# Performance work log

Measured on AMD Instinct MI355X. Metric: run time of the kernel, lower is better.

The kernel has to match this reference:

```python
import math
import jax, jax.numpy as jnp
import numpy as np

B, T, C = 4, 2048, 1024
H = 16
HS = C // H  # head_size = 64

def setup_inputs() -> dict:
    key = jax.random.key(0)
    k1, k2, k3 = jax.random.split(key, 3)
    x = jax.random.normal(k1, (B, T, C), dtype=jnp.float32)
    W_qkv = jax.random.normal(k2, (C, 3 * C), dtype=jnp.float32) * (1.0 / math.sqrt(C))
    W_proj = jax.random.normal(k3, (C, C), dtype=jnp.float32) * (1.0 / math.sqrt(C))
    b_proj = jnp.zeros((C,), dtype=jnp.float32)
    return {"x": x, "W_qkv": W_qkv, "W_proj": W_proj, "b_proj": b_proj}

def reference(x, W_qkv, W_proj, b_proj):
    Bx, Tx, Cx = x.shape
    qkv = x @ W_qkv  # [B,T,3C]
    q, k, v = jnp.split(qkv, 3, axis=-1)
    # [B,T,C] -> [B,H,T,HS]
    def heads(t):
        return t.reshape(Bx, Tx, H, HS).transpose(0, 2, 1, 3)
    q, k, v = heads(q), heads(k), heads(v)
    scores = jnp.einsum('bhqd,bhkd->bhqk', q, k) / math.sqrt(HS)
    causal = jnp.tril(jnp.ones((Tx, Tx), dtype=bool))
    scores = jnp.where(causal, scores, -jnp.inf)
    attn = jax.nn.softmax(scores, axis=-1)
    out = jnp.einsum('bhqk,bhkd->bhqd', attn, v)  # [B,H,T,HS]
    out = out.transpose(0, 2, 1, 3).reshape(Bx, Tx, Cx)
    return out @ W_proj + b_proj
```

## Files before the change

kernel.cpp:

```cpp
#include <hip/hip_runtime.h>
#include <hip/hip_bf16.h>
#include <cstdint>
#include <cstddef>

using bf16 = __hip_bfloat16;
typedef __attribute__((ext_vector_type(8))) short short8;
typedef __attribute__((ext_vector_type(4))) float floatx4;

#define B_ 4
#define T_ 2048
#define C_ 1024
#define H_ 16
#define HS_ 64
#define BT_ (B_*T_)
#define N3C (3*C_)

#define MFMA16(a,b,c) __builtin_amdgcn_mfma_f32_16x16x32_bf16((a),(b),(c),0,0,0)

#if __has_builtin(__builtin_amdgcn_exp2f)
#define EXP2(x) __builtin_amdgcn_exp2f(x)
#else
#define EXP2(x) exp2f(x)
#endif

static __device__ __forceinline__ void gld16(const bf16* g, bf16* l) {
  __builtin_amdgcn_global_load_lds(
      (const __attribute__((address_space(1))) unsigned int*)g,
      (__attribute__((address_space(3))) unsigned int*)l, 16, 0, 0);
}

static __device__ __forceinline__ unsigned short f2bf_us(float x) {
  bf16 b = __float2bfloat16(x);
  return *(unsigned short*)&b;
}

__global__ __launch_bounds__(256)
void k_prep(const float* __restrict__ x, bf16* __restrict__ xb,
            const float* __restrict__ Wqkv, bf16* __restrict__ wqkvT,
            const float* __restrict__ Wproj, bf16* __restrict__ wprojT)
{
  const int bid = blockIdx.x, tid = threadIdx.x;
  __shared__ float tile[64][65];

  if (bid < 4096) {
    const int i = bid*256 + tid;
    const float4 v0 = ((const float4*)x)[2*i];
    const float4 v1 = ((const float4*)x)[2*i + 1];
    union { bf16 b[8]; uint4 u; } cvt;
    cvt.b[0] = __float2bfloat16(v0.x);
    cvt.b[1] = __float2bfloat16(v0.y);
    cvt.b[2] = __float2bfloat16(v0.z);
    cvt.b[3] = __float2bfloat16(v0.w);
    cvt.b[4] = __float2bfloat16(v1.x);
    cvt.b[5] = __float2bfloat16(v1.y);
    cvt.b[6] = __float2bfloat16(v1.z);
    cvt.b[7] = __float2bfloat16(v1.w);
    ((uint4*)xb)[i] = cvt.u;
    return;
  }

  const float* in; bf16* out; int N, n0, k0;
  if (bid < 4864) {
    const int j = bid - 4096;
    in = Wqkv; out = wqkvT; N = N3C;
    n0 = (j % 48) * 64; k0 = (j / 48) * 64;
  } else {
    const int j = bid - 4864;
    in = Wproj; out = wprojT; N = C_;
    n0 = (j % 16) * 64; k0 = (j / 16) * 64;
  }
  const int r = tid >> 6, c = tid & 63;
  #pragma unroll
  for (int j = 0; j < 16; ++j)
    tile[r + j*4][c] = in[(size_t)(k0 + r + j*4) * N + n0 + c];
  __syncthreads();
  #pragma unroll
  for (int j = 0; j < 16; ++j) {
    int rr = r + j*4;
    out[(size_t)(n0 + rr) * C_ + k0 + c] = __float2bfloat16(tile[c][rr]);
  }
}

template<int MODE, int NB>
__global__ __launch_bounds__(256, 2)
void k_gemm(const bf16* __restrict__ A, const bf16* __restrict__ Bt,
            int N, int K,
            bf16* __restrict__ Qb, bf16* __restrict__ Kb, bf16* __restrict__ Vt,
            float* __restrict__ Out, const float* __restrict__ bias)
{
  __shared__ __align__(16) char smem[65536];
  bf16* const sAb = (bf16*)smem;
  bf16* const sBb = (bf16*)(smem + 32768);

  const int tid  = threadIdx.x;
  const int lane = tid & 63, wave = tid >> 6;
  const int quad = lane >> 4, l16 = lane & 15;
  const int wm = wave >> 1, wn = wave & 1;

  const int g = blockIdx.x;
  const int xcd = g & 7;
  const int local = g >> 3;
  const int nb = local % NB;
  const int mb = (local / NB) * 8 + xcd;
  const int m0 = mb * 128, n0 = nb * 128;

  const int ra = tid >> 3;
  const int gc = (tid & 7) ^ (ra & 7);
  const bf16* aptr = A  + (size_t)(m0 + ra) * K + gc*8;
  const bf16* bptr = Bt + (size_t)(n0 + ra) * K + gc*8;
  const size_t rj = (size_t)32 * K;

  floatx4 acc[4][4] = {};
  const int KI = K >> 6;
  const int x7a = l16 & 7;

  for (int i = 0; i <= KI; ++i) {
    __syncthreads();
    if (i < KI) {
      const int k0 = i << 6;
      bf16* sa = sAb + (i & 1) * 8192;
      bf16* sb = sBb + (i & 1) * 8192;
      #pragma unroll
      for (int q2 = 0; q2 < 4; ++q2) {
        gld16(aptr + q2*rj + k0, sa + q2*2048 + tid*8);
        gld16(bptr + q2*rj + k0, sb + q2*2048 + tid*8);
      }
    }
    if (i == 0) continue;
    const bf16* sa = sAb + ((i-1) & 1) * 8192;
    const bf16* sb = sBb + ((i-1) & 1) * 8192;
    #pragma unroll
    for (int ks = 0; ks < 2; ++ks) {
      short8 af[4], bfm[4];
      #pragma unroll
      for (int ii = 0; ii < 4; ++ii)
        af[ii] = *(const short8*)&sa[(wm*64 + ii*16 + l16)*64 + ((ks*4 + quad) ^ x7a)*8];
      #pragma unroll
      for (int ii = 0; ii < 4; ++ii)
        bfm[ii] = *(const short8*)&sb[(wn*64 + ii*16 + l16)*64 + ((ks*4 + quad) ^ x7a)*8];
      #pragma unroll
      for (int ii = 0; ii < 4; ++ii)
        #pragma unroll
        for (int j = 0; j < 4; ++j)
          acc[ii][j] = MFMA16(af[ii], bfm[j], acc[ii][j]);
    }
  }

  if (MODE == 0 && nb >= 16) {
    __syncthreads();
    unsigned short* epi = (unsigned short*)smem;
    #pragma unroll
    for (int i = 0; i < 4; ++i) {
      const int tl = wm*64 + i*16 + quad*4;
      #pragma unroll
      for (int j = 0; j < 4; ++j) {
        const int ccl = wn*64 + j*16 + l16;
        #pragma unroll
        for (int r = 0; r < 4; ++r)
          epi[ccl*132 + tl + r] = f2bf_us(acc[i][j][r]);
      }
    }
    __syncthreads();
    const int b  = m0 >> 11;
    const int t0 = m0 & 2047;
    const int h0 = (n0 - 2*C_) >> 6;
    #pragma unroll
    for (int it = 0; it < 32; ++it) {
      const int id = it*256 + tid;
      const int tp = id & 31;
      const int rest = id >> 5;
      const int tl64 = (rest & 1) * 64;
      const int ccl = rest >> 1;
      const int k0p = tp + (tp & 16);
      const unsigned lo = epi[ccl*132 + tl64 + k0p];
      const unsigned hi = epi[ccl*132 + tl64 + k0p + 16];
      const int h = h0 + (ccl >> 6), d = ccl & 63;
      unsigned* row = (unsigned*)(Vt + ((size_t)(b*H_ + h) * HS_ + d) * T_);
      row[(t0 >> 1) + tl64/2 + tp] = lo | (hi << 16);
    }
  } else {
    #pragma unroll
    for (int i = 0; i < 4; ++i) {
      const int rowb = m0 + wm*64 + i*16 + quad*4;
      #pragma unroll
      for (int j = 0; j < 4; ++j) {
        const int col = n0 + wn*64 + j*16 + l16;
        #pragma unroll
        for (int r = 0; r < 4; ++r) {
          const float v = acc[i][j][r];
          const int rr = rowb + r;
          if (MODE == 0) {
            const int b = rr >> 11, t = rr & 2047;
            const int h = (col >> 6) & 15, d = col & 63;
            const size_t addr = (((size_t)(b*H_ + h) * T_ + t) << 6) + d;
            if (nb < 8) {
              Qb[addr] = __float2bfloat16(v * 0.18033688f);
            } else {
              Kb[addr] = __float2bfloat16(v);
            }
          } else {
            Out[(size_t)rr * N + col] = v + bias[col];
          }
        }
      }
    }
  }
}

__global__ __launch_bounds__(256, 2)
void k_attn(const bf16* __restrict__ Q, const bf16* __restrict__ K,
            const bf16* __restrict__ Vt, bf16* __restrict__ att)
{
  __shared__ bf16 kbuf[2][64*64];
  __shared__ bf16 vbuf[2][64*64];
  __shared__ bf16 pbuf[4][32*64];

  const int tid  = threadIdx.x;
  const int lane = tid & 63, wave = tid >> 6;
  const int quad = lane >> 4, l16 = lane & 15;
  const int x7 = l16 & 7;

  const int g  = blockIdx.x;
  const int bh = (g & 7) * 8 + (g >> 6);
  const int bx = (g >> 3) & 7;
  const int b = bh >> 4, h = bh & 15;

  const bf16* Qp = Q  + (size_t)bh * T_ * HS_;
  const bf16* Kp = K  + (size_t)bh * T_ * HS_;
  const bf16* Vp = Vt + (size_t)bh * HS_ * T_;

  const int qbase[2] = { (15-bx)*128 + wave*32, bx*128 + wave*32 };
  const int ntk0 = 32 - 2*bx;
  const int ntk1 = 2*bx + 2;

  short8 qf[2][2][2];
  #pragma unroll
  for (int t = 0; t < 2; ++t)
    #pragma unroll
    for (int mt = 0; mt < 2; ++mt)
      #pragma unroll
      for (int ss = 0; ss < 2; ++ss)
        qf[t][mt][ss] = *(const short8*)(Qp + (size_t)(qbase[t] + mt*16 + l16) * HS_ + ss*32 + quad*8);

  floatx4 o[2][2][4] = {};
  float lrow[2][2][4] = {};

  const bf16* kg[2]; const bf16* vg[2];
  int ldsoff[2];
  #pragma unroll
  for (int it = 0; it < 2; ++it) {
    const int c = it*256 + tid;
    const int row = c >> 3;
    const int col = (c & 7) ^ (row & 7);
    kg[it] = Kp + (size_t)row * HS_ + col*8;
    vg[it] = Vp + (size_t)row * T_ + col*8;
    ldsoff[it] = c*8;
  }

  bf16* pw = pbuf[wave];
  unsigned int* pw32 = (unsigned int*)pw;
  const int c0 = l16 >> 2;
  const int dwl = l16 & 3;

  for (int i = 0; i <= ntk0; ++i) {
    __syncthreads();
    if (i < ntk0) {
      const int stk0 = i * 64;
      bf16* kb = kbuf[i & 1];
      bf16* vb = vbuf[i & 1];
      #pragma unroll
      for (int it = 0; it < 2; ++it) {
        gld16(kg[it] + (size_t)stk0 * HS_, kb + ldsoff[it]);
        gld16(vg[it] + stk0,               vb + ldsoff[it]);
      }
    }
    if (i == 0) continue;
    const int tk  = i - 1;
    const int tk0 = tk * 64;
    const bf16* kb = kbuf[tk & 1];
    const bf16* vb = vbuf[tk & 1];

    #pragma unroll
    for (int t = 0; t < 2; ++t) {
      if (t == 1 && tk >= ntk1) break;
      if (tk0 > qbase[t] + 31) continue;

      floatx4 s[2][4] = {};
      #pragma unroll
      for (int nt = 0; nt < 4; ++nt) {
        const int key = nt*16 + l16;
        #pragma unroll
        for (int ss = 0; ss < 2; ++ss) {
          short8 kf = *(const short8*)&kb[(key*8 + ((ss*4+quad) ^ x7))*8];
          s[0][nt] = MFMA16(qf[t][0][ss], kf, s[0][nt]);
          s[1][nt] = MFMA16(qf[t][1][ss], kf, s[1][nt]);
        }
      }

      if (tk0 + 63 > qbase[t]) {
        #pragma unroll
        for (int mt = 0; mt < 2; ++mt)
          #pragma unroll
          for (int nt = 0; nt < 4; ++nt) {
            const int key = tk0 + nt*16 + l16;
            #pragma unroll
            for (int r = 0; r < 4; ++r) {
              const int qr = qbase[t] + mt*16 + quad*4 + r;
              if (key > qr) s[mt][nt][r] = -1e30f;
            }
          }
      }

      #pragma unroll
      for (int mt = 0; mt < 2; ++mt) {
        #pragma unroll
        for (int r = 0; r < 4; ++r) {
          const float p0 = EXP2(s[mt][0][r]), p1 = EXP2(s[mt][1][r]);
          const float p2 = EXP2(s[mt][2][r]), p3 = EXP2(s[mt][3][r]);
          lrow[t][mt][r] += (p0 + p1) + (p2 + p3);
          const int q = mt*16 + quad*4 + r;
          const unsigned w0 = __builtin_amdgcn_perm(__float_as_uint(p1), __float_as_uint(p0), 0x07060302u);
          const unsigned w1 = __builtin_amdgcn_perm(__float_as_uint(p3), __float_as_uint(p2), 0x07060302u);
          pw32[q*32 + (((c0 + q)     & 7) << 2) + dwl] = w0;
          pw32[q*32 + (((c0 + q + 4) & 7) << 2) + dwl] = w1;
        }
      }

      #pragma unroll
      for (int ss = 0; ss < 2; ++ss) {
        short8 pf0 = *(const short8*)&pw[l16*64      + ((4*ss + quad + l16) & 7)*8];
        short8 pf1 = *(const short8*)&pw[(16+l16)*64 + ((4*ss + quad + l16) & 7)*8];
        #pragma unroll
        for (int nd = 0; nd < 4; ++nd) {
          const int d = nd*16 + l16;
          short8 vf = *(const short8*)&vb[(d*8 + ((ss*4+quad) ^ x7))*8];
          o[t][0][nd] = MFMA16(pf0, vf, o[t][0][nd]);
          o[t][1][nd] = MFMA16(pf1, vf, o[t][1][nd]);
        }
      }
    }
  }

  #pragma unroll
  for (int t = 0; t < 2; ++t) {
    #pragma unroll
    for (int mt = 0; mt < 2; ++mt) {
      #pragma unroll
      for (int r = 0; r < 4; ++r) {
        float lsum = lrow[t][mt][r];
        lsum += __shfl_xor(lsum, 1);
        lsum += __shfl_xor(lsum, 2);
        lsum += __shfl_xor(lsum, 4);
        lsum += __shfl_xor(lsum, 8);
        const float inv = 1.0f / lsum;
        const int tt = qbase[t] + mt*16 + quad*4 + r;
        #pragma unroll
        for (int nd = 0; nd < 4; ++nd)
          att[(size_t)(b*T_ + tt) * C_ + h*64 + nd*16 + l16] =
              __float2bfloat16(o[t][mt][nd][r] * inv);
      }
    }
  }
}

extern "C" void kernel_launch(void* const* d_in, const int* in_sizes, int n_in,
                              void* d_out, int out_size, void* d_ws, size_t ws_size,
                              hipStream_t stream) {
  const float* x     = (const float*)d_in[0];
  const float* Wqkv  = (const float*)d_in[1];
  const float* Wproj = (const float*)d_in[2];
  const float* bproj = (const float*)d_in[3];
  float* out = (float*)d_out;

  char* ws = (char*)d_ws;
  bf16* xb     = (bf16*)(ws + 0);
  bf16* wqkvT  = (bf16*)(ws + 16777216);
  bf16* wprojT = (bf16*)(ws + 23068672);
  bf16* Qb     = (bf16*)(ws + 25165824);
  bf16* Kb     = (bf16*)(ws + 41943040);
  bf16* Vt     = (bf16*)(ws + 58720256);
  bf16* att    = (bf16*)(ws + 75497472);

  k_prep<<<dim3(5120), 256, 0, stream>>>(x, xb, Wqkv, wqkvT, Wproj, wprojT);
  k_gemm<0, 24><<<dim3(1536), 256, 0, stream>>>(
      xb, wqkvT, N3C, C_, Qb, Kb, Vt, nullptr, nullptr);
  k_attn<<<dim3(512), 256, 0, stream>>>(Qb, Kb, Vt, att);
  k_gemm<1, 8><<<dim3(512), 256, 0, stream>>>(
      att, wprojT, C_, C_, nullptr, nullptr, nullptr, out, bproj);
}
```

Baseline: 234.7 us.

## Split paired causal attention tiles into one tile per block, heaviest first

The attention kernel previously gave each block two paired query tiles (one long, one short) to balance causal work. Now each block handles a single 128-row query tile, the grid doubles to 1024 blocks, and blocks are ordered so the longest tiles are scheduled first. Register state is halved, so launch bounds are raised to allow three blocks per CU, and s_setprio wraps the MFMA sections to favour matrix issue across waves. The risk is more K/V reloads across blocks and tail imbalance if the heavy-first ordering does not hold in hardware scheduling.

```diff
diff --git a/kernel.cpp b/kernel.cpp
--- a/kernel.cpp
+++ b/kernel.cpp
@@ -207,7 +207,7 @@
   }
 }
 
-__global__ __launch_bounds__(256, 2)
+__global__ __launch_bounds__(256, 3)
 void k_attn(const bf16* __restrict__ Q, const bf16* __restrict__ K,
             const bf16* __restrict__ Vt, bf16* __restrict__ att)
 {
@@ -221,29 +221,26 @@
   const int x7 = l16 & 7;
 
   const int g  = blockIdx.x;
-  const int bh = (g & 7) * 8 + (g >> 6);
-  const int bx = (g >> 3) & 7;
+  const int bh = (g & 7) * 8 + ((g >> 3) & 7);
+  const int qt = 15 - (g >> 6);
   const int b = bh >> 4, h = bh & 15;
 
   const bf16* Qp = Q  + (size_t)bh * T_ * HS_;
   const bf16* Kp = K  + (size_t)bh * T_ * HS_;
   const bf16* Vp = Vt + (size_t)bh * HS_ * T_;
 
-  const int qbase[2] = { (15-bx)*128 + wave*32, bx*128 + wave*32 };
-  const int ntk0 = 32 - 2*bx;
-  const int ntk1 = 2*bx + 2;
-
-  short8 qf[2][2][2];
-  #pragma unroll
-  for (int t = 0; t < 2; ++t)
-    #pragma unroll
-    for (int mt = 0; mt < 2; ++mt)
-      #pragma unroll
-      for (int ss = 0; ss < 2; ++ss)
-        qf[t][mt][ss] = *(const short8*)(Qp + (size_t)(qbase[t] + mt*16 + l16) * HS_ + ss*32 + quad*8);
-
-  floatx4 o[2][2][4] = {};
-  float lrow[2][2][4] = {};
+  const int qbase = qt*128 + wave*32;
+  const int ntk = 2*qt + 2;
+
+  short8 qf[2][2];
+  #pragma unroll
+  for (int mt = 0; mt < 2; ++mt)
+    #pragma unroll
+    for (int ss = 0; ss < 2; ++ss)
+      qf[mt][ss] = *(const short8*)(Qp + (size_t)(qbase + mt*16 + l16) * HS_ + ss*32 + quad*8);
+
+  floatx4 o[2][4] = {};
+  float lrow[2][4] = {};
 
   const bf16* kg[2]; const bf16* vg[2];
   int ldsoff[2];
@@ -262,9 +259,9 @@
   const int c0 = l16 >> 2;
   const int dwl = l16 & 3;
 
-  for (int i = 0; i <= ntk0; ++i) {
+  for (int i = 0; i <= ntk; ++i) {
     __syncthreads();
-    if (i < ntk0) {
+    if (i < ntk) {
       const int stk0 = i * 64;
       bf16* kb = kbuf[i & 1];
       bf16* vb = vbuf[i & 1];
@@ -277,88 +274,84 @@
     if (i == 0) continue;
     const int tk  = i - 1;
     const int tk0 = tk * 64;
+    if (tk0 > qbase + 31) continue;
     const bf16* kb = kbuf[tk & 1];
     const bf16* vb = vbuf[tk & 1];
 
-    #pragma unroll
-    for (int t = 0; t < 2; ++t) {
-      if (t == 1 && tk >= ntk1) break;
-      if (tk0 > qbase[t] + 31) continue;
-
-      floatx4 s[2][4] = {};
-      #pragma unroll
-      for (int nt = 0; nt < 4; ++nt) {
-        const int key = nt*16 + l16;
+    floatx4 s[2][4] = {};
+    __builtin_amdgcn_s_setprio(1);
+    #pragma unroll
+    for (int nt = 0; nt < 4; ++nt) {
+      const int key = nt*16 + l16;
+      #pragma unroll
+      for (int ss = 0; ss < 2; ++ss) {
+        short8 kf = *(const short8*)&kb[(key*8 + ((ss*4+quad) ^ x7))*8];
+        s[0][nt] = MFMA16(qf[0][ss], kf, s[0][nt]);
+        s[1][nt] = MFMA16(qf[1][ss], kf, s[1][nt]);
+      }
+    }
+    __builtin_amdgcn_s_setprio(0);
+
+    if (tk0 + 63 > qbase) {
+      #pragma unroll
+      for (int mt = 0; mt < 2; ++mt)
         #pragma unroll
-        for (int ss = 0; ss < 2; ++ss) {
-          short8 kf = *(const short8*)&kb[(key*8 + ((ss*4+quad) ^ x7))*8];
-          s[0][nt] = MFMA16(qf[t][0][ss], kf, s[0][nt]);
-          s[1][nt] = MFMA16(qf[t][1][ss], kf, s[1][nt]);
+        for (int nt = 0; nt < 4; ++nt) {
+          const int key = tk0 + nt*16 + l16;
+          #pragma unroll
+          for (int r = 0; r < 4; ++r) {
+            const int qr = qbase + mt*16 + quad*4 + r;
+            if (key > qr) s[mt][nt][r] = -1e30f;
+          }
         }
-      }
-
-      if (tk0 + 63 > qbase[t]) {
-        #pragma unroll
-        for (int mt = 0; mt < 2; ++mt)
-          #pragma unroll
-          for (int nt = 0; nt < 4; ++nt) {
-            const int key = tk0 + nt*16 + l16;
-            #pragma unroll
-            for (int r = 0; r < 4; ++r) {
-              const int qr = qbase[t] + mt*16 + quad*4 + r;
-              if (key > qr) s[mt][nt][r] = -1e30f;
-            }
-          }
-      }
-
-      #pragma unroll
-      for (int mt = 0; mt < 2; ++mt) {
-        #pragma unroll
-        for (int r = 0; r < 4; ++r) {
-          const float p0 = EXP2(s[mt][0][r]), p1 = EXP2(s[mt][1][r]);
-          const float p2 = EXP2(s[mt][2][r]), p3 = EXP2(s[mt][3][r]);
-          lrow[t][mt][r] += (p0 + p1) + (p2 + p3);
-          const int q = mt*16 + quad*4 + r;
-          const unsigned w0 = __builtin_amdgcn_perm(__float_as_uint(p1), __float_as_uint(p0), 0x07060302u);
-          const unsigned w1 = __builtin_amdgcn_perm(__float_as_uint(p3), __float_as_uint(p2), 0x07060302u);
-          pw32[q*32 + (((c0 + q)     & 7) << 2) + dwl] = w0;
-          pw32[q*32 + (((c0 + q + 4) & 7) << 2) + dwl] = w1;
-        }
-      }
-
-      #pragma unroll
-      for (int ss = 0; ss < 2; ++ss) {
-        short8 pf0 = *(const short8*)&pw[l16*64      + ((4*ss + quad + l16) & 7)*8];
-        short8 pf1 = *(const short8*)&pw[(16+l16)*64 + ((4*ss + quad + l16) & 7)*8];
-        #pragma unroll
-        for (int nd = 0; nd < 4; ++nd) {
-          const int d = nd*16 + l16;
-          short8 vf = *(const short8*)&vb[(d*8 + ((ss*4+quad) ^ x7))*8];
-          o[t][0][nd] = MFMA16(pf0, vf, o[t][0][nd]);
-          o[t][1][nd] = MFMA16(pf1, vf, o[t][1][nd]);
-        }
-      }
-    }
-  }
-
-  #pragma unroll
-  for (int t = 0; t < 2; ++t) {
+    }
+
     #pragma unroll
     for (int mt = 0; mt < 2; ++mt) {
       #pragma unroll
       for (int r = 0; r < 4; ++r) {
-        float lsum = lrow[t][mt][r];
-        lsum += __shfl_xor(lsum, 1);
-        lsum += __shfl_xor(lsum, 2);
-        lsum += __shfl_xor(lsum, 4);
-        lsum += __shfl_xor(lsum, 8);
-        const float inv = 1.0f / lsum;
-        const int tt = qbase[t] + mt*16 + quad*4 + r;
-        #pragma unroll
-        for (int nd = 0; nd < 4; ++nd)
-          att[(size_t)(b*T_ + tt) * C_ + h*64 + nd*16 + l16] =
-              __float2bfloat16(o[t][mt][nd][r] * inv);
-      }
+        const float p0 = EXP2(s[mt][0][r]), p1 = EXP2(s[mt][1][r]);
+        const float p2 = EXP2(s[mt][2][r]), p3 = EXP2(s[mt][3][r]);
+        lrow[mt][r] += (p0 + p1) + (p2 + p3);
+        const int q = mt*16 + quad*4 + r;
+        const unsigned w0 = __builtin_amdgcn_perm(__float_as_uint(p1), __float_as_uint(p0), 0x07060302u);
+        const unsigned w1 = __builtin_amdgcn_perm(__float_as_uint(p3), __float_as_uint(p2), 0x07060302u);
+        pw32[q*32 + (((c0 + q)     & 7) << 2) + dwl] = w0;
+        pw32[q*32 + (((c0 + q + 4) & 7) << 2) + dwl] = w1;
+      }
+    }
+
+    __builtin_amdgcn_s_setprio(1);
+    #pragma unroll
+    for (int ss = 0; ss < 2; ++ss) {
+      short8 pf0 = *(const short8*)&pw[l16*64      + ((4*ss + quad + l16) & 7)*8];
+      short8 pf1 = *(const short8*)&pw[(16+l16)*64 + ((4*ss + quad + l16) & 7)*8];
+      #pragma unroll
+      for (int nd = 0; nd < 4; ++nd) {
+        const int d = nd*16 + l16;
+        short8 vf = *(const short8*)&vb[(d*8 + ((ss*4+quad) ^ x7))*8];
+        o[0][nd] = MFMA16(pf0, vf, o[0][nd]);
+        o[1][nd] = MFMA16(pf1, vf, o[1][nd]);
+      }
+    }
+    __builtin_amdgcn_s_setprio(0);
+  }
+
+  #pragma unroll
+  for (int mt = 0; mt < 2; ++mt) {
+    #pragma unroll
+    for (int r = 0; r < 4; ++r) {
+      float lsum = lrow[mt][r];
+      lsum += __shfl_xor(lsum, 1);
+      lsum += __shfl_xor(lsum, 2);
+      lsum += __shfl_xor(lsum, 4);
+      lsum += __shfl_xor(lsum, 8);
+      const float inv = 1.0f / lsum;
+      const int tt = qbase + mt*16 + quad*4 + r;
+      #pragma unroll
+      for (int nd = 0; nd < 4; ++nd)
+        att[(size_t)(b*T_ + tt) * C_ + h*64 + nd*16 + l16] =
+            __float2bfloat16(o[mt][nd][r] * inv);
     }
   }
 }
@@ -384,7 +377,7 @@
   k_prep<<<dim3(5120), 256, 0, stream>>>(x, xb, Wqkv, wqkvT, Wproj, wprojT);
   k_gemm<0, 24><<<dim3(1536), 256, 0, stream>>>(
       xb, wqkvT, N3C, C_, Qb, Kb, Vt, nullptr, nullptr);
-  k_attn<<<dim3(512), 256, 0, stream>>>(Qb, Kb, Vt, att);
+  k_attn<<<dim3(1024), 256, 0, stream>>>(Qb, Kb, Vt, att);
   k_gemm<1, 8><<<dim3(512), 256, 0, stream>>>(
       att, wprojT, C_, C_, nullptr, nullptr, nullptr, out, bproj);
 }
```

Measured after the change: 232.1 us. About the same (-1.1%).
